# Kernel tuning notes

Hardware: AMD Instinct MI355X
Metric: run time of the kernel (lower is better)

## Reference

```python
import jax, jax.numpy as jnp
import numpy as np

B, S, H, D, E = 4, 1024, 1024, 4096, 8  # batch, seq, hidden, expert_dim, num_experts


def setup_inputs() -> dict:
    key = jax.random.key(0)
    ks = jax.random.split(key, 12)
    def init(k, shape, fan_in):
        return jax.random.normal(k, shape, jnp.float32) / np.float32(np.sqrt(fan_in))
    return {
        'x':  jax.random.normal(ks[0], (B, S, H), jnp.float32),
        # single-head self-attention params
        'Wq': init(ks[1], (H, H), H), 'bq': jnp.zeros((H,), jnp.float32),
        'Wk': init(ks[2], (H, H), H), 'bk': jnp.zeros((H,), jnp.float32),
        'Wv': init(ks[3], (H, H), H), 'bv': jnp.zeros((H,), jnp.float32),
        'Wo': init(ks[4], (H, H), H), 'bo': jnp.zeros((H,), jnp.float32),
        # SOME (soft mixture-of-experts) params
        'Wg': init(ks[5], (H, E), H), 'bg': jnp.zeros((E,), jnp.float32),
        'W1': init(ks[6], (E, H, D), H), 'b1': jnp.zeros((E, D), jnp.float32),
        'W2': init(ks[7], (E, D, H), D), 'b2': jnp.zeros((E, H), jnp.float32),
    }


def reference(x, Wq, bq, Wk, bk, Wv, bv, Wo, bo, Wg, bg, W1, b1, W2, b2):
    # --- TinySelfAttention (single head) + residual ---
    q = x @ Wq + bq                                   # [B,S,H]
    k = x @ Wk + bk
    v = x @ Wv + bv
    scale = jnp.asarray(1.0 / np.sqrt(H), x.dtype)
    scores = jnp.einsum('bqh,bkh->bqk', q, k) * scale  # [B,S,S]
    attn = jax.nn.softmax(scores, axis=-1)
    a = jnp.einsum('bqk,bkh->bqh', attn, v) @ Wo + bo
    x = x + a
    # --- per-token SOMEBlock (scan over seq in original == batched here) ---
    gates = jax.nn.softmax(x @ Wg + bg, axis=-1)       # [B,S,E]
    hmid = jax.nn.relu(jnp.einsum('bsh,ehd->bsed', x, W1) + b1)  # [B,S,E,D]
    eout = jnp.einsum('bsed,edh->bseh', hmid, W2) + b2            # [B,S,E,H]
    y = jnp.einsum('bse,bseh->bsh', gates, eout)                  # [B,S,H]
    return x + y
```

## Files before the change

### kernel.cpp

```cpp
#include <hip/hip_runtime.h>
#include <stdint.h>

typedef __bf16 bf16_t;
typedef __bf16 bf16x8 __attribute__((ext_vector_type(8)));
typedef __bf16 bf16x4 __attribute__((ext_vector_type(4)));
typedef float  f32x4  __attribute__((ext_vector_type(4)));

enum { M_PLAIN=0, M_BIAS, M_BIAS_RES, M_SCORES, M_W1, M_PART };

__device__ __forceinline__ void gll16(const void* g, void* l) {
    __builtin_amdgcn_global_load_lds(
        (const __attribute__((address_space(1))) void*)g,
        (__attribute__((address_space(3))) void*)l,
        16, 0, 0);
}

#define BAR()   __builtin_amdgcn_s_barrier()
#define SCHED0() __builtin_amdgcn_sched_barrier(0)
#define LGK0()  do { asm volatile("s_waitcnt lgkmcnt(0)" ::: "memory"); SCHED0(); } while(0)
#define VMC2()  do { asm volatile("s_waitcnt vmcnt(2)" ::: "memory"); SCHED0(); } while(0)
#define PRIO1() __builtin_amdgcn_s_setprio(1)
#define PRIO0() __builtin_amdgcn_s_setprio(0)

template<int MODE>
__global__ __launch_bounds__(512, 2)
void gemm256(const bf16_t* __restrict__ A, const bf16_t* __restrict__ Bt,
             bf16_t* __restrict__ Ob, float* __restrict__ Of,
             const float* __restrict__ bias, const float* __restrict__ gates,
             int ge, int einit, int zsBias, int KC, int lda, int ldb, int ldc,
             long zsA, long zsB, long zsC)
{
    __shared__ char lds[131072];

    const int z = blockIdx.z;
    A  += (long)z * zsA;
    Bt += (long)z * zsB;

    const int tid  = threadIdx.x;
    const int wave = tid >> 6, lane = tid & 63;
    const int l16  = lane & 15, quad = lane >> 4;
    const int wr = wave >> 2, wc = wave & 3;

    int bx = blockIdx.x, by = blockIdx.y;
    {
        const int gx = gridDim.x, gy = gridDim.y;
        const int nwg = gx * gy;
        if ((nwg & 7) == 0) {
            const int q   = nwg >> 3;
            const int bid = bx + gx * by;
            const int xcd = bid & 7, li = bid >> 3;
            const int cw  = (gx >= 16) ? 16 : gx;
            const int ch  = q / cw;
            if (cw * ch == q && ch > 0 && (gx % cw) == 0 && (gy % ch) == 0) {
                const int ncx = gx / cw;
                bx = (xcd % ncx) * cw + (li % cw);
                by = (xcd / ncx) * ch + (li / cw);
            }
        }
    }
    const int m0 = by * 256, n0 = bx * 256;

    const int srow = (wave << 3) + (lane >> 3);
    const int scol = ((lane & 7) * 8) ^ (((lane >> 5) & 1) << 4);
    const bf16_t* gA0 = A  + (long)(m0 +       srow) * lda + scol;
    const bf16_t* gA1 = A  + (long)(m0 + 128 + srow) * lda + scol;
    const bf16_t* gB0 = Bt + (long)(n0 +       srow) * ldb + scol;
    const bf16_t* gB1 = Bt + (long)(n0 + 128 + srow) * ldb + scol;

    const int NT = KC >> 6;
    const int NP = NT >> 1;

    auto stage = [&](int u, int d, int tt) {
        const long k0 = (long)((tt < NT ? tt : NT - 1) << 6);
        const bf16_t* g; long ldx;
        if      (u == 0) { g = gA0; ldx = lda; }
        else if (u == 1) { g = gA1; ldx = lda; }
        else if (u == 2) { g = gB0; ldx = ldb; }
        else             { g = gB1; ldx = ldb; }
        char* l = lds + (d * 4 + u) * 16384 + wave * 1024;
        gll16(g + k0, l);
        gll16(g + k0 + 64 * ldx, l + 8192);
    };

    const int vCol = (quad * 16) ^ (((l16 >> 2) & 1) << 5);
    const char* rdA = lds + l16 * 128 + vCol;
    const char* rdB = lds + (wc & 1) * 8192 + l16 * 128 + vCol;

    bf16x8 aE[8], aO[8], b0[4], b1[4];

    auto readA = [&](int qm, int d, bf16x8* dst) {
        const char* base = rdA + (d * 4 + wr) * 16384 + qm * 64 * 128;
        #pragma unroll
        for (int ii = 0; ii < 4; ii++)
            #pragma unroll
            for (int ks = 0; ks < 2; ks++)
                dst[ii * 2 + ks] = *(const bf16x8*)(base + ii * 16 * 128 + ks * 64);
    };
    auto readB = [&](int qn, int d, bf16x8* dst) {
        const char* base = rdB + (d * 4 + 2 + (wc >> 1)) * 16384 + qn * 32 * 128;
        #pragma unroll
        for (int jj = 0; jj < 2; jj++)
            #pragma unroll
            for (int ks = 0; ks < 2; ks++)
                dst[jj * 2 + ks] = *(const bf16x8*)(base + jj * 16 * 128 + ks * 64);
    };

    f32x4 acc[8][4];
    #pragma unroll
    for (int i = 0; i < 8; i++)
        #pragma unroll
        for (int j = 0; j < 4; j++)
            acc[i][j] = f32x4{0.f, 0.f, 0.f, 0.f};

    auto mfmaQ = [&](int qm, int qn, const bf16x8* aR, const bf16x8* bR) {
        PRIO1();
        #pragma unroll
        for (int ii = 0; ii < 4; ii++)
            #pragma unroll
            for (int jj = 0; jj < 2; jj++)
                #pragma unroll
                for (int ks = 0; ks < 2; ks++)
                    acc[qm * 4 + ii][qn * 2 + jj] =
                        __builtin_amdgcn_mfma_f32_16x16x32_bf16(
                            aR[ii * 2 + ks], bR[jj * 2 + ks],
                            acc[qm * 4 + ii][qn * 2 + jj], 0, 0, 0);
        PRIO0();
    };

    stage(0, 0, 0); stage(1, 0, 0); stage(2, 0, 0); stage(3, 0, 0);
    stage(0, 1, 1);
    VMC2();
    BAR(); SCHED0();
    readA(0, 0, aE); readB(0, 0, b0);

    for (int p = 0; p < NP; ++p) {
        const int t1 = 2 * p + 1, t2 = 2 * p + 2, t3 = 2 * p + 3;
        readB(1, 0, b1);  stage(1, 1, t1);  BAR(); LGK0(); mfmaQ(0, 0, aE, b0); BAR();
        readA(1, 0, aO);  stage(2, 1, t1);  BAR(); LGK0(); mfmaQ(0, 1, aE, b1); BAR();
                          stage(3, 1, t1);  BAR(); LGK0(); mfmaQ(1, 0, aO, b0); BAR();
        stage(0, 0, t2); VMC2(); BAR(); SCHED0();
        readA(0, 1, aE); readB(0, 1, b0); LGK0(); mfmaQ(1, 1, aO, b1); BAR();
        readB(1, 1, b1);  stage(1, 0, t2);  BAR(); LGK0(); mfmaQ(0, 0, aE, b0); BAR();
        readA(1, 1, aO);  stage(2, 0, t2);  BAR(); LGK0(); mfmaQ(0, 1, aE, b1); BAR();
                          stage(3, 0, t2);  BAR(); LGK0(); mfmaQ(1, 0, aO, b0); BAR();
        stage(0, 1, t3); VMC2(); BAR(); SCHED0();
        readA(0, 0, aE); readB(0, 0, b0); LGK0(); mfmaQ(1, 1, aO, b1); BAR();
    }

    #pragma unroll
    for (int i = 0; i < 8; i++) {
        const int row = m0 + wr * 128 + i * 16 + quad * 4;
        #pragma unroll
        for (int j = 0; j < 4; j++) {
            const int col = n0 + wc * 64 + j * 16 + l16;
            #pragma unroll
            for (int r = 0; r < 4; r++) {
                const int rr = row + r;
                const long idx = (long)z * zsC + (long)rr * ldc + col;
                const float vv = acc[i][j][r];
                if (MODE == M_BIAS) {
                    Ob[idx] = (bf16_t)(vv + bias[z * zsBias + col]);
                } else if (MODE == M_W1) {
                    float t = vv + bias[z * zsBias + col];
                    t = t > 0.f ? t : 0.f;
                    Ob[idx] = (bf16_t)(t * gates[rr * 8 + (ge >= 0 ? ge : z)]);
                } else if (MODE == M_PART) {
                    Of[idx] = einit ? vv : (Of[idx] + vv);
                }
            }
        }
    }
}

template<int MODE>
__global__ __launch_bounds__(256)
void gemm_nt(const bf16_t* __restrict__ A, const bf16_t* __restrict__ Bt,
             bf16_t* __restrict__ Ob, float* __restrict__ Of,
             const float* __restrict__ bias, const float* __restrict__ res,
             const float* __restrict__ gates, int ge, int einit, float scale,
             int KC, int lda, int ldb, int ldc, int zsCol,
             long zsA, long zsB, long zsC)
{
    __shared__ bf16_t As[2][128 * 32];
    __shared__ bf16_t Bs[2][128 * 32];

    const int z = blockIdx.z;
    A  += (long)z * zsA;
    Bt += (long)z * zsB;

    const int tid  = threadIdx.x;
    const int wave = tid >> 6, lane = tid & 63;
    const int l16  = lane & 15, quad = lane >> 4;

    int bx = blockIdx.x, by = blockIdx.y;
    {
        const int gx = gridDim.x, gy = gridDim.y;
        const int nwg = gx * gy;
        if ((nwg & 7) == 0) {
            const int q   = nwg >> 3;
            const int bid = bx + gx * by;
            const int xcd = bid & 7, li = bid >> 3;
            const int cw  = (gx >= 16) ? 16 : gx;
            const int ch  = q / cw;
            if (cw * ch == q && ch > 0 && (gx % cw) == 0 && (gy % ch) == 0) {
                const int ncx = gx / cw;
                bx = (xcd % ncx) * cw + (li % cw);
                by = (xcd / ncx) * ch + (li / cw);
            }
        }
    }
    const int m0 = by * 128, n0 = bx * 128;
    const int wr = wave >> 1, wc = wave & 1;

    const int srow = wave * 16 + (lane >> 2);
    const int scol = (lane & 3) * 8;
    const bf16_t* gA0 = A  + (long)(m0 + srow) * lda + scol;
    const bf16_t* gA1 = A  + (long)(m0 + 64 + srow) * lda + scol;
    const bf16_t* gB0 = Bt + (long)(n0 + srow) * ldb + scol;
    const bf16_t* gB1 = Bt + (long)(n0 + 64 + srow) * ldb + scol;

    auto stage = [&](int t, int b) {
        const int k0 = t << 5;
        gll16(gA0 + k0, &As[b][wave * 512]);
        gll16(gA1 + k0, &As[b][2048 + wave * 512]);
        gll16(gB0 + k0, &Bs[b][wave * 512]);
        gll16(gB1 + k0, &Bs[b][2048 + wave * 512]);
    };

    f32x4 acc[4][4];
    #pragma unroll
    for (int i = 0; i < 4; i++)
        #pragma unroll
        for (int j = 0; j < 4; j++)
            acc[i][j] = f32x4{0.f, 0.f, 0.f, 0.f};

    const int nst = KC >> 5;
    stage(0, 0);
    for (int t = 0; t < nst; ++t) {
        const int cur = t & 1;
        if (t + 1 < nst) {
            stage(t + 1, cur ^ 1);
            asm volatile("s_waitcnt vmcnt(4)" ::: "memory");
        } else {
            asm volatile("s_waitcnt vmcnt(0)" ::: "memory");
        }
        __builtin_amdgcn_s_barrier();
        asm volatile("" ::: "memory");

        bf16x8 af[4], bfr[4];
        #pragma unroll
        for (int i = 0; i < 4; i++)
            af[i] = *(const bf16x8*)&As[cur][(wr * 64 + i * 16 + l16) * 32 + quad * 8];
        #pragma unroll
        for (int j = 0; j < 4; j++)
            bfr[j] = *(const bf16x8*)&Bs[cur][(wc * 64 + j * 16 + l16) * 32 + quad * 8];

        #pragma unroll
        for (int i = 0; i < 4; i++)
            #pragma unroll
            for (int j = 0; j < 4; j++)
                acc[i][j] = __builtin_amdgcn_mfma_f32_16x16x32_bf16(af[i], bfr[j], acc[i][j], 0, 0, 0);

        asm volatile("" ::: "memory");
        __builtin_amdgcn_s_barrier();
    }

    #pragma unroll
    for (int i = 0; i < 4; i++) {
        const int row = m0 + wr * 64 + i * 16 + quad * 4;
        #pragma unroll
        for (int j = 0; j < 4; j++) {
            const int col = n0 + wc * 64 + j * 16 + l16;
            #pragma unroll
            for (int r = 0; r < 4; r++) {
                const int rr = row + r;
                const long idx = (long)z * zsC + (long)rr * ldc + (long)z * zsCol + col;
                const float vv = acc[i][j][r];
                if (MODE == M_SCORES) {
                    Of[idx] = vv * scale;
                } else if (MODE == M_PLAIN) {
                    Ob[idx] = (bf16_t)vv;
                } else if (MODE == M_BIAS) {
                    Ob[idx] = (bf16_t)(vv + bias[col]);
                } else if (MODE == M_BIAS_RES) {
                    Ob[idx] = (bf16_t)(vv + bias[col] + res[idx]);
                } else if (MODE == M_PART) {
                    Of[idx] = einit ? vv : (Of[idx] + vv);
                }
            }
        }
    }
}

template<typename TIN>
__global__ __launch_bounds__(256)
void transpose_to_bf16(const TIN* __restrict__ in, bf16_t* __restrict__ out,
                       int C, int ldOut, int zcol, long sIn, long sOut)
{
    __shared__ bf16_t tile[32][33];
    const int z = blockIdx.z;
    in  += (long)z * sIn;
    out += (long)z * sOut + (long)z * zcol;
    const int c0 = blockIdx.x * 32, r0 = blockIdx.y * 32;
    const int tx = threadIdx.x, ty = threadIdx.y;
    #pragma unroll
    for (int i = ty; i < 32; i += 8)
        tile[i][tx] = (bf16_t)(float)in[(long)(r0 + i) * C + c0 + tx];
    __syncthreads();
    #pragma unroll
    for (int i = ty; i < 32; i += 8)
        out[(long)(c0 + i) * ldOut + r0 + tx] = tile[tx][i];
}

__global__ __launch_bounds__(256)
void convert_f32_bf16(const float* __restrict__ in, bf16_t* __restrict__ out, int n)
{
    const int i = (blockIdx.x * 256 + threadIdx.x) * 4;
    if (i >= n) return;
    const float4 v = *(const float4*)(in + i);
    bf16x4 o;
    o[0] = (bf16_t)v.x; o[1] = (bf16_t)v.y; o[2] = (bf16_t)v.z; o[3] = (bf16_t)v.w;
    *(bf16x4*)(out + i) = o;
}

__global__ __launch_bounds__(256)
void softmax_rows(const float* __restrict__ Sc, bf16_t* __restrict__ P)
{
    const int row = blockIdx.x, tid = threadIdx.x, wave = tid >> 6, lane = tid & 63;
    const float* sr = Sc + (long)row * 1024;
    bf16_t* pr = P + (long)row * 1024;
    float v[4];
    float mx = -3.4e38f;
    #pragma unroll
    for (int i = 0; i < 4; i++) { v[i] = sr[tid + 256 * i]; mx = fmaxf(mx, v[i]); }
    #pragma unroll
    for (int off = 32; off; off >>= 1) mx = fmaxf(mx, __shfl_down(mx, off));
    __shared__ float sm[4], ss[4];
    if (lane == 0) sm[wave] = mx;
    __syncthreads();
    mx = fmaxf(fmaxf(sm[0], sm[1]), fmaxf(sm[2], sm[3]));
    float sum = 0.f;
    #pragma unroll
    for (int i = 0; i < 4; i++) { v[i] = __expf(v[i] - mx); sum += v[i]; }
    #pragma unroll
    for (int off = 32; off; off >>= 1) sum += __shfl_down(sum, off);
    if (lane == 0) ss[wave] = sum;
    __syncthreads();
    const float inv = 1.f / (ss[0] + ss[1] + ss[2] + ss[3]);
    #pragma unroll
    for (int i = 0; i < 4; i++) pr[tid + 256 * i] = (bf16_t)(v[i] * inv);
}

__global__ __launch_bounds__(256)
void gates_kernel(const bf16_t* __restrict__ x2, const float* __restrict__ Wg,
                  const float* __restrict__ bg, float* __restrict__ gates, int H)
{
    const int wave = threadIdx.x >> 6, lane = threadIdx.x & 63;
    const int t = blockIdx.x * 4 + wave;
    const bf16_t* xr = x2 + (long)t * H;
    float acc[8] = {0.f, 0.f, 0.f, 0.f, 0.f, 0.f, 0.f, 0.f};
    for (int h = lane; h < H; h += 64) {
        const float xv = (float)xr[h];
        const float4 w0 = *(const float4*)(Wg + h * 8);
        const float4 w1 = *(const float4*)(Wg + h * 8 + 4);
        acc[0] += xv * w0.x; acc[1] += xv * w0.y; acc[2] += xv * w0.z; acc[3] += xv * w0.w;
        acc[4] += xv * w1.x; acc[5] += xv * w1.y; acc[6] += xv * w1.z; acc[7] += xv * w1.w;
    }
    #pragma unroll
    for (int off = 32; off; off >>= 1)
        #pragma unroll
        for (int e = 0; e < 8; e++) acc[e] += __shfl_down(acc[e], off);
    if (lane == 0) {
        float mx = -3.4e38f;
        #pragma unroll
        for (int e = 0; e < 8; e++) { acc[e] += bg[e]; mx = fmaxf(mx, acc[e]); }
        float s = 0.f;
        #pragma unroll
        for (int e = 0; e < 8; e++) { acc[e] = __expf(acc[e] - mx); s += acc[e]; }
        const float inv = 1.f / s;
        #pragma unroll
        for (int e = 0; e < 8; e++) gates[t * 8 + e] = acc[e] * inv;
    }
}

__global__ __launch_bounds__(256)
void final_add(const bf16_t* __restrict__ x2, const float* __restrict__ yp,
               const float* __restrict__ gates, const float* __restrict__ b2,
               float* __restrict__ out, long TH)
{
    const long i = (blockIdx.x * 256L + threadIdx.x) * 4;
    const int t = (int)(i >> 10), h = (int)(i & 1023);
    const float4 a0 = *(const float4*)(yp + i);
    const float4 a1 = *(const float4*)(yp + TH + i);
    const float4 a2 = *(const float4*)(yp + 2 * TH + i);
    const float4 a3 = *(const float4*)(yp + 3 * TH + i);
    float sx = a0.x + a1.x + a2.x + a3.x;
    float sy = a0.y + a1.y + a2.y + a3.y;
    float sz = a0.z + a1.z + a2.z + a3.z;
    float sw = a0.w + a1.w + a2.w + a3.w;
    const float* g = gates + t * 8;
    #pragma unroll
    for (int e = 0; e < 8; e++) {
        const float ge = g[e];
        const float4 b = *(const float4*)(b2 + e * 1024 + h);
        sx += ge * b.x; sy += ge * b.y; sz += ge * b.z; sw += ge * b.w;
    }
    const bf16x4 xv = *(const bf16x4*)(x2 + i);
    float4 o;
    o.x = (float)xv[0] + sx;
    o.y = (float)xv[1] + sy;
    o.z = (float)xv[2] + sz;
    o.w = (float)xv[3] + sw;
    *(float4*)(out + i) = o;
}

extern "C" void kernel_launch(void* const* d_in, const int* in_sizes, int n_in,
                              void* d_out, int out_size, void* d_ws, size_t ws_size,
                              hipStream_t stream)
{
    const int S = 1024, H = 1024, D = 4096, T = 4096;
    const long TH = (long)T * H;

    const float* x  = (const float*)d_in[0];
    const float* Wq = (const float*)d_in[1];
    const float* bq = (const float*)d_in[2];
    const float* Wk = (const float*)d_in[3];
    const float* bk = (const float*)d_in[4];
    const float* Wv = (const float*)d_in[5];
    const float* bv = (const float*)d_in[6];
    const float* Wo = (const float*)d_in[7];
    const float* bo = (const float*)d_in[8];
    const float* Wg = (const float*)d_in[9];
    const float* bg = (const float*)d_in[10];
    const float* W1 = (const float*)d_in[11];
    const float* b1 = (const float*)d_in[12];
    const float* W2 = (const float*)d_in[13];
    const float* b2 = (const float*)d_in[14];
    float* out = (float*)d_out;

    char* base = (char*)d_ws;
    float*  yp     = (float*) (base + 0);
    bf16_t* x_bf   = (bf16_t*)(base + 0);
    bf16_t* WqT    = (bf16_t*)(base + 8388608);
    bf16_t* WkT    = (bf16_t*)(base + 10485760);
    bf16_t* WvT    = (bf16_t*)(base + 12582912);
    bf16_t* WoT    = (bf16_t*)(base + 14680064);
    bf16_t* qkv    = (bf16_t*)(base + 16777216);
    bf16_t* attn   = (bf16_t*)(base + 16777216);
    bf16_t* a      = (bf16_t*)(base + 25165824);
    bf16_t* vT     = (bf16_t*)(base + 41943040);
    float*  scores = (float*) (base + 50331648);
    bf16_t* x2     = (bf16_t*)(base + 67108864);
    float*  gates  = (float*) (base + 75497472);
    float*  bqkv   = (float*) (base + 75628544);
    bf16_t* W1T    = (bf16_t*)(base + 75640832);
    bf16_t* hmid   = (bf16_t*)(base + 142749696);
    bf16_t* W2T    = (bf16_t*)(base + 411185152);

    const dim3 tb(32, 8);

    convert_f32_bf16<<<4096, 256, 0, stream>>>(x, x_bf, T * H);
    transpose_to_bf16<float><<<dim3(32, 32, 1), tb, 0, stream>>>(Wq, WqT, H, H, 0, 0, 0);
    transpose_to_bf16<float><<<dim3(32, 32, 1), tb, 0, stream>>>(Wk, WkT, H, H, 0, 0, 0);
    transpose_to_bf16<float><<<dim3(32, 32, 1), tb, 0, stream>>>(Wv, WvT, H, H, 0, 0, 0);
    transpose_to_bf16<float><<<dim3(32, 32, 1), tb, 0, stream>>>(Wo, WoT, H, H, 0, 0, 0);
    hipMemcpyAsync(bqkv,        bq, H * sizeof(float), hipMemcpyDeviceToDevice, stream);
    hipMemcpyAsync(bqkv + 1024, bk, H * sizeof(float), hipMemcpyDeviceToDevice, stream);
    hipMemcpyAsync(bqkv + 2048, bv, H * sizeof(float), hipMemcpyDeviceToDevice, stream);

    gemm256<M_BIAS><<<dim3(12, 16, 1), 512, 0, stream>>>(x_bf, WqT, qkv, nullptr, bqkv, nullptr, -1, 0, 0,
                                                         H, H, H, 3072, 0, 0, 0);
    transpose_to_bf16<bf16_t><<<dim3(32, 32, 4), tb, 0, stream>>>(qkv + 2048, vT, 3072, S, 0, (long)S * 3072, (long)H * S);

    gemm_nt<M_SCORES><<<dim3(8, 8, 4), 256, 0, stream>>>(qkv, qkv + 1024, nullptr, scores, nullptr, nullptr, nullptr, -1, 0, 0.03125f,
                                                         H, 3072, 3072, S, 0, (long)S * 3072, (long)S * 3072, (long)S * S);
    softmax_rows<<<4096, 256, 0, stream>>>(scores, attn);

    gemm_nt<M_PLAIN><<<dim3(8, 8, 4), 256, 0, stream>>>(attn, vT, a, nullptr, nullptr, nullptr, nullptr, -1, 0, 0.f,
                                                        S, S, S, H, 0, (long)S * S, (long)H * S, (long)S * H);
    gemm_nt<M_BIAS_RES><<<dim3(8, 32, 1), 256, 0, stream>>>(a, WoT, x2, nullptr, bo, x, nullptr, -1, 0, 0.f,
                                                            H, H, H, H, 0, 0, 0, 0);

    gates_kernel<<<1024, 256, 0, stream>>>(x2, Wg, bg, gates, H);

    transpose_to_bf16<float><<<dim3(128, 32, 8), tb, 0, stream>>>(W1, W1T, D, H, 0, (long)H * D, (long)D * H);
    gemm256<M_W1><<<dim3(16, 16, 8), 512, 0, stream>>>(x2, W1T, hmid, nullptr, b1, gates, -1, 0, D,
                                                       H, H, H, 32768, 0, (long)D * H, 4096);
    transpose_to_bf16<float><<<dim3(32, 128, 8), tb, 0, stream>>>(W2, W2T, H, 32768, 4096, (long)D * H, 0);
    gemm256<M_PART><<<dim3(4, 16, 4), 512, 0, stream>>>(hmid, W2T, nullptr, yp, nullptr, nullptr, -1, 1, 0,
                                                        8192, 32768, 32768, H, 8192, 8192, TH);

    final_add<<<4096, 256, 0, stream>>>(x2, yp, gates, b2, out, TH);
}
```

Baseline: 1.137 ms.

## Route attention GEMMs through 256x256 kernel and use full XOR LDS swizzle

```diff
diff --git a/kernel.cpp b/kernel.cpp
--- a/kernel.cpp
+++ b/kernel.cpp
@@ -26,8 +26,10 @@
 __global__ __launch_bounds__(512, 2)
 void gemm256(const bf16_t* __restrict__ A, const bf16_t* __restrict__ Bt,
              bf16_t* __restrict__ Ob, float* __restrict__ Of,
-             const float* __restrict__ bias, const float* __restrict__ gates,
-             int ge, int einit, int zsBias, int KC, int lda, int ldb, int ldc,
+             const float* __restrict__ bias, const float* __restrict__ res,
+             const float* __restrict__ gates,
+             int ge, int einit, int zsBias, float scale,
+             int KC, int lda, int ldb, int ldc,
              long zsA, long zsB, long zsC)
 {
     __shared__ char lds[131072];
@@ -61,7 +63,7 @@
     const int m0 = by * 256, n0 = bx * 256;
 
     const int srow = (wave << 3) + (lane >> 3);
-    const int scol = ((lane & 7) * 8) ^ (((lane >> 5) & 1) << 4);
+    const int scol = (((lane & 7) ^ ((lane >> 3) & 7)) * 8);
     const bf16_t* gA0 = A  + (long)(m0 +       srow) * lda + scol;
     const bf16_t* gA1 = A  + (long)(m0 + 128 + srow) * lda + scol;
     const bf16_t* gB0 = Bt + (long)(n0 +       srow) * ldb + scol;
@@ -82,27 +84,28 @@
         gll16(g + k0 + 64 * ldx, l + 8192);
     };
 
-    const int vCol = (quad * 16) ^ (((l16 >> 2) & 1) << 5);
-    const char* rdA = lds + l16 * 128 + vCol;
-    const char* rdB = lds + (wc & 1) * 8192 + l16 * 128 + vCol;
+    const int xr = l16 & 7;
+    const int o0 = ((quad ^ (xr & 3)) << 4) | ((xr >> 2) << 6);
+    const int o1 = o0 ^ 64;
 
     bf16x8 aE[8], aO[8], b0[4], b1[4];
 
     auto readA = [&](int qm, int d, bf16x8* dst) {
-        const char* base = rdA + (d * 4 + wr) * 16384 + qm * 64 * 128;
-        #pragma unroll
-        for (int ii = 0; ii < 4; ii++)
-            #pragma unroll
-            for (int ks = 0; ks < 2; ks++)
-                dst[ii * 2 + ks] = *(const bf16x8*)(base + ii * 16 * 128 + ks * 64);
+        const char* base = lds + (d * 4 + wr) * 16384 + qm * 64 * 128 + l16 * 128;
+        #pragma unroll
+        for (int ii = 0; ii < 4; ii++) {
+            dst[ii * 2 + 0] = *(const bf16x8*)(base + ii * 2048 + o0);
+            dst[ii * 2 + 1] = *(const bf16x8*)(base + ii * 2048 + o1);
+        }
     };
     auto readB = [&](int qn, int d, bf16x8* dst) {
-        const char* base = rdB + (d * 4 + 2 + (wc >> 1)) * 16384 + qn * 32 * 128;
-        #pragma unroll
-        for (int jj = 0; jj < 2; jj++)
-            #pragma unroll
-            for (int ks = 0; ks < 2; ks++)
-                dst[jj * 2 + ks] = *(const bf16x8*)(base + jj * 16 * 128 + ks * 64);
+        const char* base = lds + (d * 4 + 2 + (wc >> 1)) * 16384 + (wc & 1) * 8192
+                         + qn * 32 * 128 + l16 * 128;
+        #pragma unroll
+        for (int jj = 0; jj < 2; jj++) {
+            dst[jj * 2 + 0] = *(const bf16x8*)(base + jj * 2048 + o0);
+            dst[jj * 2 + 1] = *(const bf16x8*)(base + jj * 2048 + o1);
+        }
     };
 
     f32x4 acc[8][4];
@@ -158,132 +161,18 @@
                 const int rr = row + r;
                 const long idx = (long)z * zsC + (long)rr * ldc + col;
                 const float vv = acc[i][j][r];
-                if (MODE == M_BIAS) {
+                if (MODE == M_PLAIN) {
+                    Ob[idx] = (bf16_t)vv;
+                } else if (MODE == M_BIAS) {
                     Ob[idx] = (bf16_t)(vv + bias[z * zsBias + col]);
+                } else if (MODE == M_BIAS_RES) {
+                    Ob[idx] = (bf16_t)(vv + bias[col] + res[idx]);
+                } else if (MODE == M_SCORES) {
+                    Of[idx] = vv * scale;
                 } else if (MODE == M_W1) {
                     float t = vv + bias[z * zsBias + col];
                     t = t > 0.f ? t : 0.f;
                     Ob[idx] = (bf16_t)(t * gates[rr * 8 + (ge >= 0 ? ge : z)]);
-                } else if (MODE == M_PART) {
-                    Of[idx] = einit ? vv : (Of[idx] + vv);
-                }
-            }
-        }
-    }
-}
-
-template<int MODE>
-__global__ __launch_bounds__(256)
-void gemm_nt(const bf16_t* __restrict__ A, const bf16_t* __restrict__ Bt,
-             bf16_t* __restrict__ Ob, float* __restrict__ Of,
-             const float* __restrict__ bias, const float* __restrict__ res,
-             const float* __restrict__ gates, int ge, int einit, float scale,
-             int KC, int lda, int ldb, int ldc, int zsCol,
-             long zsA, long zsB, long zsC)
-{
-    __shared__ bf16_t As[2][128 * 32];
-    __shared__ bf16_t Bs[2][128 * 32];
-
-    const int z = blockIdx.z;
-    A  += (long)z * zsA;
-    Bt += (long)z * zsB;
-
-    const int tid  = threadIdx.x;
-    const int wave = tid >> 6, lane = tid & 63;
-    const int l16  = lane & 15, quad = lane >> 4;
-
-    int bx = blockIdx.x, by = blockIdx.y;
-    {
-        const int gx = gridDim.x, gy = gridDim.y;
-        const int nwg = gx * gy;
-        if ((nwg & 7) == 0) {
-            const int q   = nwg >> 3;
-            const int bid = bx + gx * by;
-            const int xcd = bid & 7, li = bid >> 3;
-            const int cw  = (gx >= 16) ? 16 : gx;
-            const int ch  = q / cw;
-            if (cw * ch == q && ch > 0 && (gx % cw) == 0 && (gy % ch) == 0) {
-                const int ncx = gx / cw;
-                bx = (xcd % ncx) * cw + (li % cw);
-                by = (xcd / ncx) * ch + (li / cw);
-            }
-        }
-    }
-    const int m0 = by * 128, n0 = bx * 128;
-    const int wr = wave >> 1, wc = wave & 1;
-
-    const int srow = wave * 16 + (lane >> 2);
-    const int scol = (lane & 3) * 8;
-    const bf16_t* gA0 = A  + (long)(m0 + srow) * lda + scol;
-    const bf16_t* gA1 = A  + (long)(m0 + 64 + srow) * lda + scol;
-    const bf16_t* gB0 = Bt + (long)(n0 + srow) * ldb + scol;
-    const bf16_t* gB1 = Bt + (long)(n0 + 64 + srow) * ldb + scol;
-
-    auto stage = [&](int t, int b) {
-        const int k0 = t << 5;
-        gll16(gA0 + k0, &As[b][wave * 512]);
-        gll16(gA1 + k0, &As[b][2048 + wave * 512]);
-        gll16(gB0 + k0, &Bs[b][wave * 512]);
-        gll16(gB1 + k0, &Bs[b][2048 + wave * 512]);
-    };
-
-    f32x4 acc[4][4];
-    #pragma unroll
-    for (int i = 0; i < 4; i++)
-        #pragma unroll
-        for (int j = 0; j < 4; j++)
-            acc[i][j] = f32x4{0.f, 0.f, 0.f, 0.f};
-
-    const int nst = KC >> 5;
-    stage(0, 0);
-    for (int t = 0; t < nst; ++t) {
-        const int cur = t & 1;
-        if (t + 1 < nst) {
-            stage(t + 1, cur ^ 1);
-            asm volatile("s_waitcnt vmcnt(4)" ::: "memory");
-        } else {
-            asm volatile("s_waitcnt vmcnt(0)" ::: "memory");
-        }
-        __builtin_amdgcn_s_barrier();
-        asm volatile("" ::: "memory");
-
-        bf16x8 af[4], bfr[4];
-        #pragma unroll
-        for (int i = 0; i < 4; i++)
-            af[i] = *(const bf16x8*)&As[cur][(wr * 64 + i * 16 + l16) * 32 + quad * 8];
-        #pragma unroll
-        for (int j = 0; j < 4; j++)
-            bfr[j] = *(const bf16x8*)&Bs[cur][(wc * 64 + j * 16 + l16) * 32 + quad * 8];
-
-        #pragma unroll
-        for (int i = 0; i < 4; i++)
-            #pragma unroll
-            for (int j = 0; j < 4; j++)
-                acc[i][j] = __builtin_amdgcn_mfma_f32_16x16x32_bf16(af[i], bfr[j], acc[i][j], 0, 0, 0);
-
-        asm volatile("" ::: "memory");
-        __builtin_amdgcn_s_barrier();
-    }
-
-    #pragma unroll
-    for (int i = 0; i < 4; i++) {
-        const int row = m0 + wr * 64 + i * 16 + quad * 4;
-        #pragma unroll
-        for (int j = 0; j < 4; j++) {
-            const int col = n0 + wc * 64 + j * 16 + l16;
-            #pragma unroll
-            for (int r = 0; r < 4; r++) {
-                const int rr = row + r;
-                const long idx = (long)z * zsC + (long)rr * ldc + (long)z * zsCol + col;
-                const float vv = acc[i][j][r];
-                if (MODE == M_SCORES) {
-                    Of[idx] = vv * scale;
-                } else if (MODE == M_PLAIN) {
-                    Ob[idx] = (bf16_t)vv;
-                } else if (MODE == M_BIAS) {
-                    Ob[idx] = (bf16_t)(vv + bias[col]);
-                } else if (MODE == M_BIAS_RES) {
-                    Ob[idx] = (bf16_t)(vv + bias[col] + res[idx]);
                 } else if (MODE == M_PART) {
                     Of[idx] = einit ? vv : (Of[idx] + vv);
                 }
@@ -468,27 +357,29 @@
     hipMemcpyAsync(bqkv + 1024, bk, H * sizeof(float), hipMemcpyDeviceToDevice, stream);
     hipMemcpyAsync(bqkv + 2048, bv, H * sizeof(float), hipMemcpyDeviceToDevice, stream);
 
-    gemm256<M_BIAS><<<dim3(12, 16, 1), 512, 0, stream>>>(x_bf, WqT, qkv, nullptr, bqkv, nullptr, -1, 0, 0,
-                                                         H, H, H, 3072, 0, 0, 0);
+    gemm256<M_BIAS><<<dim3(12, 16, 1), 512, 0, stream>>>(x_bf, WqT, qkv, nullptr, bqkv, nullptr, nullptr,
+                                                         -1, 0, 0, 0.f, H, H, H, 3072, 0, 0, 0);
     transpose_to_bf16<bf16_t><<<dim3(32, 32, 4), tb, 0, stream>>>(qkv + 2048, vT, 3072, S, 0, (long)S * 3072, (long)H * S);
 
-    gemm_nt<M_SCORES><<<dim3(8, 8, 4), 256, 0, stream>>>(qkv, qkv + 1024, nullptr, scores, nullptr, nullptr, nullptr, -1, 0, 0.03125f,
-                                                         H, 3072, 3072, S, 0, (long)S * 3072, (long)S * 3072, (long)S * S);
+    gemm256<M_SCORES><<<dim3(4, 4, 4), 512, 0, stream>>>(qkv, qkv + 1024, nullptr, scores, nullptr, nullptr, nullptr,
+                                                         -1, 0, 0, 0.03125f, H, 3072, 3072, S,
+                                                         (long)S * 3072, (long)S * 3072, (long)S * S);
     softmax_rows<<<4096, 256, 0, stream>>>(scores, attn);
 
-    gemm_nt<M_PLAIN><<<dim3(8, 8, 4), 256, 0, stream>>>(attn, vT, a, nullptr, nullptr, nullptr, nullptr, -1, 0, 0.f,
-                                                        S, S, S, H, 0, (long)S * S, (long)H * S, (long)S * H);
-    gemm_nt<M_BIAS_RES><<<dim3(8, 32, 1), 256, 0, stream>>>(a, WoT, x2, nullptr, bo, x, nullptr, -1, 0, 0.f,
-                                                            H, H, H, H, 0, 0, 0, 0);
+    gemm256<M_PLAIN><<<dim3(4, 4, 4), 512, 0, stream>>>(attn, vT, a, nullptr, nullptr, nullptr, nullptr,
+                                                        -1, 0, 0, 0.f, S, S, S, H,
+                                                        (long)S * S, (long)H * S, (long)S * H);
+    gemm256<M_BIAS_RES><<<dim3(4, 16, 1), 512, 0, stream>>>(a, WoT, x2, nullptr, bo, x, nullptr,
+                                                            -1, 0, 0, 0.f, H, H, H, H, 0, 0, 0);
 
     gates_kernel<<<1024, 256, 0, stream>>>(x2, Wg, bg, gates, H);
 
     transpose_to_bf16<float><<<dim3(128, 32, 8), tb, 0, stream>>>(W1, W1T, D, H, 0, (long)H * D, (long)D * H);
-    gemm256<M_W1><<<dim3(16, 16, 8), 512, 0, stream>>>(x2, W1T, hmid, nullptr, b1, gates, -1, 0, D,
-                                                       H, H, H, 32768, 0, (long)D * H, 4096);
+    gemm256<M_W1><<<dim3(16, 16, 8), 512, 0, stream>>>(x2, W1T, hmid, nullptr, b1, nullptr, gates,
+                                                       -1, 0, D, 0.f, H, H, H, 32768, 0, (long)D * H, 4096);
     transpose_to_bf16<float><<<dim3(32, 128, 8), tb, 0, stream>>>(W2, W2T, H, 32768, 4096, (long)D * H, 0);
-    gemm256<M_PART><<<dim3(4, 16, 4), 512, 0, stream>>>(hmid, W2T, nullptr, yp, nullptr, nullptr, -1, 1, 0,
-                                                        8192, 32768, 32768, H, 8192, 8192, TH);
+    gemm256<M_PART><<<dim3(4, 16, 4), 512, 0, stream>>>(hmid, W2T, nullptr, yp, nullptr, nullptr, nullptr,
+                                                        -1, 1, 0, 0.f, 8192, 32768, 32768, H, 8192, 8192, TH);
 
     final_add<<<4096, 256, 0, stream>>>(x2, yp, gates, b2, out, TH);
 }
```

After: 1.087 ms. -4.4%, faster.
